# Performance work log

Measured on AMD Instinct MI355X. Metric: run time of the kernel, lower is better.

The kernel has to match this reference:

```python
import jax, jax.numpy as jnp
import numpy as np

N = 50000   # nodes
E = 800000  # edges
G = 64      # graphs in batch
H1, D1 = 2, 64   # gat1: 2 heads x 64
D2 = 32          # gat2: 1 head x 32
IN = 1
EPS = 1e-5


def _gat(h, src, dst, W, al, ar, Wres, bias, Hh, D):
    # DGL GATConv (eval mode): project, per-edge attention, edge softmax over dst, scatter-sum, residual + bias
    feat = (h @ W).reshape(N, Hh, D)                     # [N,H,D]
    el = jnp.sum(feat * al, axis=-1)                     # [N,H]
    er = jnp.sum(feat * ar, axis=-1)                     # [N,H]
    e = jax.nn.leaky_relu(el[src] + er[dst], 0.2)        # [E,H]
    m = jax.ops.segment_max(e, dst, num_segments=N)      # [N,H] (stable softmax)
    a = jnp.exp(e - m[dst])
    s = jax.ops.segment_sum(a, dst, num_segments=N)
    alpha = a / s[dst]                                   # [E,H]
    msg = feat[src] * alpha[:, :, None]                  # [E,H,D]
    rst = jax.ops.segment_sum(msg, dst, num_segments=N)  # [N,H,D]
    res = (h @ Wres).reshape(N, Hh, D)
    return rst + res + bias.reshape(1, Hh, D)


def _bn(x, gamma, beta, mean, var):
    return (x - mean) * jax.lax.rsqrt(var + EPS) * gamma + beta


def setup_inputs() -> dict:
    key = jax.random.key(0)
    ks = jax.random.split(key, 32)
    rn = lambda i, shape: jax.random.normal(ks[i], shape, jnp.float32) * 0.1
    inp = {
        'feat': jax.random.normal(ks[0], (N, IN), jnp.float32),
        'W1': rn(1, (IN, H1 * D1)), 'al1': rn(2, (H1, D1)), 'ar1': rn(3, (H1, D1)),
        'res1': rn(4, (IN, H1 * D1)), 'b1': rn(5, (H1 * D1,)),
        'g1_gamma': jnp.ones((H1 * D1,), jnp.float32), 'g1_beta': jnp.zeros((H1 * D1,), jnp.float32),
        'g1_mean': rn(6, (H1 * D1,)), 'g1_var': jax.random.uniform(ks[7], (H1 * D1,), jnp.float32) + 0.5,
        'W2': rn(8, (H1 * D1, D2)), 'al2': rn(9, (1, D2)), 'ar2': rn(10, (1, D2)),
        'res2': rn(11, (H1 * D1, D2)), 'b2': rn(12, (D2,)),
        'g2_gamma': jnp.ones((D2,), jnp.float32), 'g2_beta': jnp.zeros((D2,), jnp.float32),
        'g2_mean': rn(13, (D2,)), 'g2_var': jax.random.uniform(ks[14], (D2,), jnp.float32) + 0.5,
        'Wd1': rn(15, (D2, H1 * D1)), 'bd1': rn(16, (H1 * D1,)),
        'gd_gamma': jnp.ones((H1 * D1,), jnp.float32), 'gd_beta': jnp.zeros((H1 * D1,), jnp.float32),
        'gd_mean': rn(17, (H1 * D1,)), 'gd_var': jax.random.uniform(ks[18], (H1 * D1,), jnp.float32) + 0.5,
        'Wd2': rn(19, (H1 * D1, IN)), 'bd2': rn(20, (IN,)),
        'src': jax.random.randint(ks[21], (E,), 0, N, jnp.int32),
        'dst': jax.random.randint(ks[22], (E,), 0, N, jnp.int32),
        'graph_ids': jnp.sort(jax.random.randint(ks[23], (N,), 0, G, jnp.int32)),
    }
    return inp


def reference(feat, W1, al1, ar1, res1, b1, g1_gamma, g1_beta, g1_mean, g1_var,
              W2, al2, ar2, res2, b2, g2_gamma, g2_beta, g2_mean, g2_var,
              Wd1, bd1, gd_gamma, gd_beta, gd_mean, gd_var, Wd2, bd2,
              src, dst, graph_ids):
    h = _gat(feat, src, dst, W1, al1, ar1, res1, b1, H1, D1)   # [N,2,64]
    h = h.reshape(N, H1 * D1)
    h = jax.nn.relu(_bn(h, g1_gamma, g1_beta, g1_mean, g1_var))
    h = _gat(h, src, dst, W2, al2, ar2, res2, b2, 1, D2)       # [N,1,32]
    h = h.reshape(N, D2)
    h = jax.nn.relu(_bn(h, g2_gamma, g2_beta, g2_mean, g2_var))
    # dgl.mean_nodes over batched graphs
    counts = jax.ops.segment_sum(jnp.ones((N,), h.dtype), graph_ids, num_segments=G)
    graph_rep = jax.ops.segment_sum(h, graph_ids, num_segments=G) / jnp.maximum(counts, 1.0)[:, None]
    # decoder: Linear -> BN -> ReLU -> Linear (dropout off in eval)
    d = jax.nn.relu(_bn(h @ Wd1 + bd1, gd_gamma, gd_beta, gd_mean, gd_var))
    reconstruction = d @ Wd2 + bd2
    return graph_rep, reconstruction
```

## Files before the change

kernel.cpp:

```cpp
#include <hip/hip_runtime.h>
#include <hip/hip_bf16.h>
#include <hip/hip_fp16.h>

#define NN 50000
#define NE 800000
#define NG 64
#define C1 128
#define D2 32
#define CAP 32
#define RNG 6250
#define NCH 391
#define BN_EPS 1e-5f
#define PREP_BLOCKS 2048

#define CST_A   0
#define CST_B   2
#define CST_P   4
#define CST_Q   132
#define CST_R   260
#define CST_SC2 388
#define CST_RC2 420
#define CST_SD  452
#define CST_RD  580
#define CST_N   1024

#define UO_DEGP  0
#define UO_OVFC  800000
#define UO_WK    800016
#define ZERO_UNITS 800144
#define UO_FLAG  800144
#define UO_CST   800160
#define UO_ESRC2 801184
#define UO_OVF   1601184
#define UO_FCAN  3201184
#define UO_F2    3251184
#define UO_RS2   4051184
#define UO_EL2   5651184
#define UO_ER2   5701184
#define UO_END   5751184

typedef _Float16 h2vec __attribute__((ext_vector_type(2)));

__device__ __forceinline__ float lrelu(float x) { return fmaxf(x, 0.2f * x); }
__device__ __forceinline__ float bu2f(unsigned int u) {
    union { unsigned int i; float f; } v; v.i = (u & 0xFFFFu) << 16; return v.f;
}
__device__ __forceinline__ unsigned short f2bu(float f) {
    union { float f; unsigned int i; } v; v.f = f;
    unsigned int r = v.i + 0x7FFFu + ((v.i >> 16) & 1u);
    return (unsigned short)(r >> 16);
}
__device__ __forceinline__ unsigned int packh2(float a, float b) {
    h2vec h; h.x = (_Float16)a; h.y = (_Float16)b;
    union { h2vec h; unsigned int u; } v; v.h = h; return v.u;
}
__device__ __forceinline__ h2vec as_h2(unsigned int u) {
    union { unsigned int u; h2vec h; } v; v.u = u; return v.h;
}
__device__ __forceinline__ float ldw(const void* p, int i, int bf) {
    return bf ? bu2f(((const unsigned short*)p)[i]) : ((const float*)p)[i];
}
__device__ __forceinline__ int sniff64(const unsigned int* fw, int l) {
    int cnt = 0;
    for (int j = l; j < 256; j += 64) {
        unsigned int b = (fw[j] >> 8) & 0x7Fu;
        cnt += (b >= 0x3Au && b <= 0x41u) ? 1 : 0;
    }
#pragma unroll
    for (int m = 32; m >= 1; m >>= 1) cnt += __shfl_xor(cnt, m);
    return (cnt > 128) ? 1 : 0;
}

__global__ __launch_bounds__(256) void k_prep(
                       const void* __restrict__ feat, const int* __restrict__ dst,
                       const int* __restrict__ src,
                       float* __restrict__ fcan, int* __restrict__ degp,
                       unsigned short* __restrict__ esrc2,
                       int2* __restrict__ ovf, int* __restrict__ ovfc,
                       int* __restrict__ wk,
                       const void* W1, const void* al1, const void* ar1,
                       const void* res1, const void* b1,
                       const void* g1g, const void* g1b, const void* g1m, const void* g1v,
                       const void* b2v, const void* g2g, const void* g2b,
                       const void* g2m, const void* g2v,
                       const void* bd1, const void* gdg, const void* gdb,
                       const void* gdm, const void* gdv,
                       int* __restrict__ flag, float* __restrict__ cst) {
    __shared__ int sBf;
    __shared__ int sC;
    int t = threadIdx.x;
    if (t < 64) {
        int b = sniff64((const unsigned int*)feat, t);
        if (t == 0) sBf = b;
    }
    __syncthreads();
    int bf = sBf;

    if (blockIdx.x == 0) {
        if (t == 0) *flag = bf;
        if (t < 128) {
            if (t < 2) {
                float a = 0.0f, b = 0.0f;
                for (int d = 0; d < 64; ++d) {
                    float w = ldw(W1, t * 64 + d, bf);
                    a += w * ldw(al1, t * 64 + d, bf);
                    b += w * ldw(ar1, t * 64 + d, bf);
                }
                cst[CST_A + t] = a;
                cst[CST_B + t] = b;
            }
            {
                float sc = rsqrtf(ldw(g1v, t, bf) + BN_EPS) * ldw(g1g, t, bf);
                cst[CST_P + t] = ldw(W1, t, bf) * sc;
                cst[CST_Q + t] = ldw(res1, t, bf) * sc;
                cst[CST_R + t] = (ldw(b1, t, bf) - ldw(g1m, t, bf)) * sc + ldw(g1b, t, bf);
            }
            if (t < D2) {
                float sc = rsqrtf(ldw(g2v, t, bf) + BN_EPS) * ldw(g2g, t, bf);
                cst[CST_SC2 + t] = sc;
                cst[CST_RC2 + t] = (ldw(b2v, t, bf) - ldw(g2m, t, bf)) * sc + ldw(g2b, t, bf);
            }
            {
                float sc = rsqrtf(ldw(gdv, t, bf) + BN_EPS) * ldw(gdg, t, bf);
                cst[CST_SD + t] = sc;
                cst[CST_RD + t] = (ldw(bd1, t, bf) - ldw(gdm, t, bf)) * sc + ldw(gdb, t, bf);
            }
        }
    }

    for (int k = blockIdx.x * 256 + t; k < NN; k += PREP_BLOCKS * 256)
        fcan[k] = ldw(feat, k, bf);

    int xcc;
    asm volatile("s_getreg_b32 %0, hwreg(HW_REG_XCC_ID)" : "=s"(xcc));
    xcc &= 7;

    for (int rr = 0; rr < 8; ++rr) {
        int r = (xcc + rr) & 7;
        int lo = r * RNG, hi = lo + RNG;
        for (;;) {
            if (t == 0) sC = atomicAdd(&wk[r * 16], 1);
            __syncthreads();
            int c = sC;
            __syncthreads();
            if (c >= NCH) break;
#pragma unroll
            for (int j = 0; j < 8; ++j) {
                int k = c * 2048 + j * 256 + t;
                if (k < NE) {
                    int d = dst[k];
                    if (d >= lo && d < hi) {
                        int slot = atomicAdd(&degp[d << 4], 1);
                        if (slot < CAP) {
                            esrc2[d * CAP + slot] = (unsigned short)src[k];
                        } else {
                            int p = atomicAdd(ovfc, 1);
                            ovf[p] = make_int2(d, src[k]);
                        }
                    }
                }
            }
        }
    }
}

__global__ __launch_bounds__(256) void k_layer1(
        const float* __restrict__ fcan, const void* W2, const void* res2,
        const void* al2, const void* ar2,
        const int* __restrict__ flag, const float* __restrict__ cst,
        const int* __restrict__ degp, const unsigned short* __restrict__ esrc2,
        const int2* __restrict__ ovf, const int* __restrict__ ovfc,
        unsigned short* __restrict__ F2, float* __restrict__ RS2,
        float* __restrict__ EL2, float* __restrict__ ER2) {
    __shared__ unsigned int sW2pk[32 * 66];
    __shared__ unsigned int sR2pk[32 * 66];
    __shared__ unsigned int sH1pk[32 * 66];
    __shared__ float sP[C1], sQ[C1], sR[C1];
    __shared__ float sAl[D2], sAr[D2];
    int t = threadIdx.x;
    int bf = *flag;
    for (int u = t; u < 2048; u += 256) {
        int cw = u >> 5, l2 = u & 31;
        sW2pk[l2 * 66 + cw] = packh2(ldw(W2, cw * D2 + l2, bf),
                                     ldw(W2, (cw + 64) * D2 + l2, bf));
        sR2pk[l2 * 66 + cw] = packh2(ldw(res2, cw * D2 + l2, bf),
                                     ldw(res2, (cw + 64) * D2 + l2, bf));
    }
    if (t < C1) { sP[t] = cst[CST_P + t]; sQ[t] = cst[CST_Q + t]; sR[t] = cst[CST_R + t]; }
    if (t < D2) { sAl[t] = ldw(al2, t, bf); sAr[t] = ldw(ar2, t, bf); }
    __syncthreads();

    int l = t & 31;
    int g = t >> 5;
    int base = blockIdx.x * 32;
    float A0 = cst[CST_A + 0], A1 = cst[CST_A + 1];
    float B0 = cst[CST_B + 0], B1 = cst[CST_B + 1];

    int dcap[4], draw[4];
    float fiK[4];
#pragma unroll
    for (int k = 0; k < 4; ++k) {
        int i = base + g * 4 + k;
        if (i < NN) {
            draw[k] = degp[i << 4];
            dcap[k] = draw[k] < CAP ? draw[k] : CAP;
            fiK[k] = fcan[i];
        } else { draw[k] = 0; dcap[k] = 0; fiK[k] = 0.0f; }
    }
    float S0[4], S1[4], N0[4], N1[4];
#pragma unroll
    for (int k = 0; k < 4; ++k) { S0[k] = S1[k] = N0[k] = N1[k] = 0.0f; }
    int sA[4];
#pragma unroll
    for (int k = 0; k < 4; ++k)
        sA[k] = (l < dcap[k]) ? (int)esrc2[(base + g * 4 + k) * CAP + l] : 0;
    float fA[4];
#pragma unroll
    for (int k = 0; k < 4; ++k) fA[k] = fcan[sA[k]];
#pragma unroll
    for (int k = 0; k < 4; ++k) {
        if (l < dcap[k]) {
            float w0 = __expf(lrelu(A0 * fA[k] + B0 * fiK[k]));
            float w1 = __expf(lrelu(A1 * fA[k] + B1 * fiK[k]));
            S0[k] += w0; N0[k] += w0 * fA[k];
            S1[k] += w1; N1[k] += w1 * fA[k];
        }
    }
#pragma unroll
    for (int k = 0; k < 4; ++k) {
        if (draw[k] > CAP) {
            int i = base + g * 4 + k;
            int novf = *ovfc;
            for (int p = l; p < novf; p += 32) {
                int2 o = ovf[p];
                if (o.x == i) {
                    float fs = fcan[o.y];
                    float w0 = __expf(lrelu(A0 * fs + B0 * fiK[k]));
                    float w1 = __expf(lrelu(A1 * fs + B1 * fiK[k]));
                    S0[k] += w0; N0[k] += w0 * fs;
                    S1[k] += w1; N1[k] += w1 * fs;
                }
            }
        }
    }
#pragma unroll
    for (int m = 16; m >= 1; m >>= 1) {
#pragma unroll
        for (int k = 0; k < 4; ++k) {
            S0[k] += __shfl_xor(S0[k], m); N0[k] += __shfl_xor(N0[k], m);
            S1[k] += __shfl_xor(S1[k], m); N1[k] += __shfl_xor(N1[k], m);
        }
    }
#pragma unroll
    for (int k = 0; k < 4; ++k) {
        int slot = g * 4 + k;
        float T0 = S0[k] > 0.0f ? N0[k] / S0[k] : 0.0f;
        float T1 = S1[k] > 0.0f ? N1[k] / S1[k] : 0.0f;
        float h0  = fmaxf(sP[l]      * T0 + sQ[l]      * fiK[k] + sR[l],      0.0f);
        float h1v = fmaxf(sP[l + 32] * T0 + sQ[l + 32] * fiK[k] + sR[l + 32], 0.0f);
        float h2v = fmaxf(sP[l + 64] * T1 + sQ[l + 64] * fiK[k] + sR[l + 64], 0.0f);
        float h3v = fmaxf(sP[l + 96] * T1 + sQ[l + 96] * fiK[k] + sR[l + 96], 0.0f);
        sH1pk[slot * 66 + l]      = packh2(h0,  h2v);
        sH1pk[slot * 66 + l + 32] = packh2(h1v, h3v);
    }
    __syncthreads();

    int w = t >> 6;
    int half = (t >> 5) & 1;
    int nb0 = w * 8 + half * 4;
    float aF[4] = {0.f, 0.f, 0.f, 0.f}, aR[4] = {0.f, 0.f, 0.f, 0.f};
    for (int cw = 0; cw < 64; cw += 2) {
        uint2 wq = *(const uint2*)&sW2pk[l * 66 + cw];
        uint2 rq = *(const uint2*)&sR2pk[l * 66 + cw];
#pragma unroll
        for (int n = 0; n < 4; ++n) {
            uint2 hq = *(const uint2*)&sH1pk[(nb0 + n) * 66 + cw];
            aF[n] = __builtin_amdgcn_fdot2(as_h2(hq.x), as_h2(wq.x),
                    __builtin_amdgcn_fdot2(as_h2(hq.y), as_h2(wq.y), aF[n], false), false);
            aR[n] = __builtin_amdgcn_fdot2(as_h2(hq.x), as_h2(rq.x),
                    __builtin_amdgcn_fdot2(as_h2(hq.y), as_h2(rq.y), aR[n], false), false);
        }
    }
#pragma unroll
    for (int n = 0; n < 4; ++n) {
        int i = base + nb0 + n;
        if (i < NN) {
            float elp = aF[n] * sAl[l], erp = aF[n] * sAr[l];
#pragma unroll
            for (int m = 16; m >= 1; m >>= 1) {
                elp += __shfl_xor(elp, m);
                erp += __shfl_xor(erp, m);
            }
            if (l == 0) { EL2[i] = elp; ER2[i] = erp; }
            F2[(size_t)i * D2 + l]  = f2bu(aF[n]);
            RS2[(size_t)i * D2 + l] = aR[n];
        }
    }
}

__global__ __launch_bounds__(256, 8) void k_final(
        const void* Wd1, const void* Wd2, const void* bd2,
        const int* __restrict__ flag, const float* __restrict__ cst,
        const int* __restrict__ degp, const unsigned short* __restrict__ esrc2,
        const int2* __restrict__ ovf, const int* __restrict__ ovfc,
        const unsigned short* __restrict__ F2, float* __restrict__ RS2,
        const float* __restrict__ EL2, const float* __restrict__ ER2,
        float* __restrict__ out) {
    __shared__ float sWd1x[4096];
    __shared__ unsigned int sWS[8 * 64];
    int t = threadIdx.x;
    int bf = *flag;
    for (int u = t; u < 4096; u += 256) {
        int d = u >> 7, lq = (u >> 2) & 31, j = u & 3;
        sWd1x[u] = ldw(Wd1, d * C1 + j * 32 + lq, bf);
    }

    int i = (blockIdx.x * 256 + t) >> 5;
    int l = t & 31;
    int nb = t >> 5;

    float sc2 = cst[CST_SC2 + l], rc2 = cst[CST_RC2 + l];
    float sd0 = cst[CST_SD + l],      rd0 = cst[CST_RD + l];
    float sd1 = cst[CST_SD + l + 32], rd1 = cst[CST_RD + l + 32];
    float sd2 = cst[CST_SD + l + 64], rd2 = cst[CST_RD + l + 64];
    float sd3 = cst[CST_SD + l + 96], rd3 = cst[CST_RD + l + 96];
    float wd2_0 = ldw(Wd2, l, bf),      wd2_1 = ldw(Wd2, l + 32, bf);
    float wd2_2 = ldw(Wd2, l + 64, bf), wd2_3 = ldw(Wd2, l + 96, bf);
    __syncthreads();

    float eri = ER2[i];
    int dr = degp[i << 4];
    int dcap = dr < CAP ? dr : CAP;
    const unsigned short* row = &esrc2[i * CAP];

    int sMy = 0; float wMy = 0.0f;
    if (l < dcap) {
        sMy = (int)row[l];
        wMy = __expf(lrelu(EL2[sMy] + eri));
    }
    float S = wMy;
#pragma unroll
    for (int m = 16; m >= 1; m >>= 1) S += __shfl_xor(S, m);
    sWS[nb * 64 + 2 * l]     = __float_as_uint(wMy);
    sWS[nb * 64 + 2 * l + 1] = (unsigned int)sMy;

    float aF0 = 0.f, aF1 = 0.f, aF2 = 0.f, aF3 = 0.f;
    int e = 0;
    for (; e + 3 < dcap; e += 4) {
        uint2 p0 = *(const uint2*)&sWS[nb * 64 + 2 * e];
        uint2 p1 = *(const uint2*)&sWS[nb * 64 + 2 * (e + 1)];
        uint2 p2 = *(const uint2*)&sWS[nb * 64 + 2 * (e + 2)];
        uint2 p3 = *(const uint2*)&sWS[nb * 64 + 2 * (e + 3)];
        float v0 = bu2f(F2[(size_t)p0.y * D2 + l]);
        float v1 = bu2f(F2[(size_t)p1.y * D2 + l]);
        float v2 = bu2f(F2[(size_t)p2.y * D2 + l]);
        float v3 = bu2f(F2[(size_t)p3.y * D2 + l]);
        aF0 = fmaf(__uint_as_float(p0.x), v0, aF0);
        aF1 = fmaf(__uint_as_float(p1.x), v1, aF1);
        aF2 = fmaf(__uint_as_float(p2.x), v2, aF2);
        aF3 = fmaf(__uint_as_float(p3.x), v3, aF3);
    }
    for (; e < dcap; ++e) {
        uint2 p = *(const uint2*)&sWS[nb * 64 + 2 * e];
        aF0 = fmaf(__uint_as_float(p.x), bu2f(F2[(size_t)p.y * D2 + l]), aF0);
    }
    if (dr > CAP) {
        int novf = *ovfc;
        for (int p = 0; p < novf; ++p) {
            int2 o = ovf[p];
            if (o.x == i) {
                float wA = __expf(lrelu(EL2[o.y] + eri));
                S += wA;
                aF0 = fmaf(wA, bu2f(F2[(size_t)o.y * D2 + l]), aF0);
            }
        }
    }
    float aF = (aF0 + aF1) + (aF2 + aF3);
    float inv = S > 0.0f ? 1.0f / S : 0.0f;

    float h2 = fmaxf((aF * inv + RS2[(size_t)i * D2 + l]) * sc2 + rc2, 0.0f);
    RS2[(size_t)i * D2 + l] = h2;

    const float4* Wx = (const float4*)sWd1x;
    float ac0 = 0.0f, ac1 = 0.0f, ac2 = 0.0f, ac3 = 0.0f;
#pragma unroll
    for (int d = 0; d < D2; ++d) {
        float h = __shfl(h2, d, 32);
        float4 wv = Wx[d * 32 + l];
        ac0 = fmaf(h, wv.x, ac0);
        ac1 = fmaf(h, wv.y, ac1);
        ac2 = fmaf(h, wv.z, ac2);
        ac3 = fmaf(h, wv.w, ac3);
    }
    float rec = fmaxf(ac0 * sd0 + rd0, 0.0f) * wd2_0
              + fmaxf(ac1 * sd1 + rd1, 0.0f) * wd2_1
              + fmaxf(ac2 * sd2 + rd2, 0.0f) * wd2_2
              + fmaxf(ac3 * sd3 + rd3, 0.0f) * wd2_3;
#pragma unroll
    for (int m = 16; m >= 1; m >>= 1) rec += __shfl_xor(rec, m);
    if (l == 0) out[NG * D2 + i] = rec + ldw(bd2, 0, bf);
}

__global__ __launch_bounds__(256) void k_pool2(const int* __restrict__ gid,
                                               const float* __restrict__ H2,
                                               float* __restrict__ out) {
    __shared__ int sLo, sHi;
    __shared__ float sAcc[32 * 32];
    int g = blockIdx.x >> 2;
    int part = blockIdx.x & 3;
    int t = threadIdx.x;
    if (t == 0) {
        int lo = 0, hi = NN;
        while (lo < hi) { int m = (lo + hi) >> 1; if (gid[m] < g) lo = m + 1; else hi = m; }
        sLo = lo;
        lo = 0; hi = NN;
        while (lo < hi) { int m = (lo + hi) >> 1; if (gid[m] < g + 1) lo = m + 1; else hi = m; }
        sHi = lo;
    }
    __syncthreads();
    int lo = sLo, hi = sHi;
    int q = t & 7;
    int row = t >> 3;
    float4 acc = make_float4(0.f, 0.f, 0.f, 0.f);
    for (int i = lo + part * 32 + row; i < hi; i += 128) {
        float4 v = ((const float4*)&H2[(size_t)i * D2])[q];
        acc.x += v.x; acc.y += v.y; acc.z += v.z; acc.w += v.w;
    }
    *(float4*)&sAcc[row * 32 + 4 * q] = acc;
    __syncthreads();
    if (t < 32) {
        float a = 0.0f;
        for (int r = 0; r < 32; ++r) a += sAcc[r * 32 + t];
        float inv = 1.0f / fmaxf((float)(hi - lo), 1.0f);
        atomicAdd(&out[g * D2 + t], a * inv);
    }
}

extern "C" void kernel_launch(void* const* d_in, const int* in_sizes, int n_in,
                              void* d_out, int out_size, void* d_ws, size_t ws_size,
                              hipStream_t stream) {
    const void* feat = d_in[0];
    const void* W1 = d_in[1];  const void* al1 = d_in[2];  const void* ar1 = d_in[3];
    const void* res1 = d_in[4]; const void* b1 = d_in[5];
    const void* g1g = d_in[6]; const void* g1b = d_in[7];
    const void* g1m = d_in[8]; const void* g1v = d_in[9];
    const void* W2 = d_in[10]; const void* al2 = d_in[11]; const void* ar2 = d_in[12];
    const void* res2 = d_in[13]; const void* b2v = d_in[14];
    const void* g2g = d_in[15]; const void* g2b = d_in[16];
    const void* g2m = d_in[17]; const void* g2v = d_in[18];
    const void* Wd1 = d_in[19]; const void* bd1 = d_in[20];
    const void* gdg = d_in[21]; const void* gdb = d_in[22];
    const void* gdm = d_in[23]; const void* gdv = d_in[24];
    const void* Wd2 = d_in[25]; const void* bd2 = d_in[26];
    const int* src = (const int*)d_in[27];
    const int* dst = (const int*)d_in[28];
    const int* gid = (const int*)d_in[29];

    unsigned int* wsu = (unsigned int*)d_ws;
    int* degp   = (int*)(wsu + UO_DEGP);
    int* ovfc   = (int*)(wsu + UO_OVFC);
    int* wk     = (int*)(wsu + UO_WK);
    int* flag   = (int*)(wsu + UO_FLAG);
    float* cst  = (float*)(wsu + UO_CST);
    unsigned short* esrc2 = (unsigned short*)(wsu + UO_ESRC2);
    int2* ovf   = (int2*)(wsu + UO_OVF);
    float* fcan = (float*)(wsu + UO_FCAN);
    unsigned short* F2 = (unsigned short*)(wsu + UO_F2);
    float* RS2  = (float*)(wsu + UO_RS2);
    float* EL2  = (float*)(wsu + UO_EL2);
    float* ER2  = (float*)(wsu + UO_ER2);

    hipMemsetAsync(d_ws, 0, (size_t)ZERO_UNITS * 4, stream);
    hipMemsetAsync(d_out, 0, (size_t)NG * D2 * sizeof(float), stream);

    k_prep<<<PREP_BLOCKS, 256, 0, stream>>>(feat, dst, src, fcan, degp,
                                            esrc2, ovf, ovfc, wk,
                                            W1, al1, ar1, res1, b1,
                                            g1g, g1b, g1m, g1v,
                                            b2v, g2g, g2b, g2m, g2v,
                                            bd1, gdg, gdb, gdm, gdv,
                                            flag, cst);

    k_layer1<<<(NN + 31) / 32, 256, 0, stream>>>(fcan, W2, res2, al2, ar2, flag, cst,
                                                 degp, esrc2, ovf, ovfc,
                                                 F2, RS2, EL2, ER2);

    k_final<<<(NN * 32) / 256, 256, 0, stream>>>(Wd1, Wd2, bd2, flag, cst,
                                                 degp, esrc2, ovf, ovfc,
                                                 F2, RS2, EL2, ER2,
                                                 (float*)d_out);

    k_pool2<<<NG * 4, 256, 0, stream>>>(gid, RS2, (float*)d_out);
}
```

Before: 284.3 us.

## Fuse all stages into one cooperative persistent kernel with grid syncs

```diff
diff --git a/kernel.cpp b/kernel.cpp
--- a/kernel.cpp
+++ b/kernel.cpp
@@ -1,6 +1,9 @@
 #include <hip/hip_runtime.h>
 #include <hip/hip_bf16.h>
 #include <hip/hip_fp16.h>
+#include <hip/hip_cooperative_groups.h>
+
+namespace cg = cooperative_groups;
 
 #define NN 50000
 #define NE 800000
@@ -11,7 +14,7 @@
 #define RNG 6250
 #define NCH 391
 #define BN_EPS 1e-5f
-#define PREP_BLOCKS 2048
+#define FGRID 1024
 
 #define CST_A   0
 #define CST_B   2
@@ -26,20 +29,38 @@
 
 #define UO_DEGP  0
 #define UO_OVFC  800000
-#define UO_WK    800016
-#define ZERO_UNITS 800144
-#define UO_FLAG  800144
-#define UO_CST   800160
-#define UO_ESRC2 801184
-#define UO_OVF   1601184
-#define UO_FCAN  3201184
-#define UO_F2    3251184
-#define UO_RS2   4051184
-#define UO_EL2   5651184
-#define UO_ER2   5701184
-#define UO_END   5751184
+#define ZERO_UNITS 800016
+#define UO_CST   800016
+#define UO_ESRC2 801040
+#define UO_OVF   1601040
+#define UO_FCAN  3201040
+#define UO_F2    3251040
+#define UO_RS2   4051040
+#define UO_EL2   5651040
+#define UO_ER2   5701040
 
 typedef _Float16 h2vec __attribute__((ext_vector_type(2)));
+
+struct Params {
+    const void *feat, *W1, *al1, *ar1, *res1, *b1, *g1g, *g1b, *g1m, *g1v;
+    const void *W2, *al2, *ar2, *res2, *b2v, *g2g, *g2b, *g2m, *g2v;
+    const void *Wd1, *bd1, *gdg, *gdb, *gdm, *gdv, *Wd2, *bd2;
+    const int *src, *dst, *gid;
+    unsigned int *wsz;
+    int *degp, *ovfc;
+    float *cst, *fcan;
+    unsigned short *esrc2;
+    int2 *ovf;
+    unsigned short *F2;
+    float *RS2, *EL2, *ER2, *out;
+};
+
+union SMem {
+    struct { unsigned int W2pk[32 * 66], R2pk[32 * 66], H1pk[32 * 66];
+             float P[C1], Q[C1], R[C1], Al[D2], Ar[D2]; } l1;
+    struct { float Wd1x[4096]; unsigned int WS[8 * 64]; } fin;
+    struct { float Acc[32 * 32]; int Lo, Hi; } pool;
+};
 
 __device__ __forceinline__ float lrelu(float x) { return fmaxf(x, 0.2f * x); }
 __device__ __forceinline__ float bu2f(unsigned int u) {
@@ -70,93 +91,51 @@
     for (int m = 32; m >= 1; m >>= 1) cnt += __shfl_xor(cnt, m);
     return (cnt > 128) ? 1 : 0;
 }
-
-__global__ __launch_bounds__(256) void k_prep(
-                       const void* __restrict__ feat, const int* __restrict__ dst,
-                       const int* __restrict__ src,
-                       float* __restrict__ fcan, int* __restrict__ degp,
-                       unsigned short* __restrict__ esrc2,
-                       int2* __restrict__ ovf, int* __restrict__ ovfc,
-                       int* __restrict__ wk,
-                       const void* W1, const void* al1, const void* ar1,
-                       const void* res1, const void* b1,
-                       const void* g1g, const void* g1b, const void* g1m, const void* g1v,
-                       const void* b2v, const void* g2g, const void* g2b,
-                       const void* g2m, const void* g2v,
-                       const void* bd1, const void* gdg, const void* gdb,
-                       const void* gdm, const void* gdv,
-                       int* __restrict__ flag, float* __restrict__ cst) {
-    __shared__ int sBf;
-    __shared__ int sC;
-    int t = threadIdx.x;
-    if (t < 64) {
-        int b = sniff64((const unsigned int*)feat, t);
-        if (t == 0) sBf = b;
-    }
+__device__ __forceinline__ int block_bf(const void* feat, int t, int* sBf) {
+    if (t < 64) { int b = sniff64((const unsigned int*)feat, t); if (t == 0) *sBf = b; }
     __syncthreads();
-    int bf = sBf;
-
-    if (blockIdx.x == 0) {
-        if (t == 0) *flag = bf;
-        if (t < 128) {
-            if (t < 2) {
-                float a = 0.0f, b = 0.0f;
-                for (int d = 0; d < 64; ++d) {
-                    float w = ldw(W1, t * 64 + d, bf);
-                    a += w * ldw(al1, t * 64 + d, bf);
-                    b += w * ldw(ar1, t * 64 + d, bf);
-                }
-                cst[CST_A + t] = a;
-                cst[CST_B + t] = b;
-            }
-            {
-                float sc = rsqrtf(ldw(g1v, t, bf) + BN_EPS) * ldw(g1g, t, bf);
-                cst[CST_P + t] = ldw(W1, t, bf) * sc;
-                cst[CST_Q + t] = ldw(res1, t, bf) * sc;
-                cst[CST_R + t] = (ldw(b1, t, bf) - ldw(g1m, t, bf)) * sc + ldw(g1b, t, bf);
-            }
-            if (t < D2) {
-                float sc = rsqrtf(ldw(g2v, t, bf) + BN_EPS) * ldw(g2g, t, bf);
-                cst[CST_SC2 + t] = sc;
-                cst[CST_RC2 + t] = (ldw(b2v, t, bf) - ldw(g2m, t, bf)) * sc + ldw(g2b, t, bf);
-            }
-            {
-                float sc = rsqrtf(ldw(gdv, t, bf) + BN_EPS) * ldw(gdg, t, bf);
-                cst[CST_SD + t] = sc;
-                cst[CST_RD + t] = (ldw(bd1, t, bf) - ldw(gdm, t, bf)) * sc + ldw(gdb, t, bf);
-            }
-        }
-    }
-
-    for (int k = blockIdx.x * 256 + t; k < NN; k += PREP_BLOCKS * 256)
-        fcan[k] = ldw(feat, k, bf);
-
-    int xcc;
-    asm volatile("s_getreg_b32 %0, hwreg(HW_REG_XCC_ID)" : "=s"(xcc));
-    xcc &= 7;
-
-    for (int rr = 0; rr < 8; ++rr) {
-        int r = (xcc + rr) & 7;
+    return *sBf;
+}
+
+__device__ __forceinline__ void dev_fold(const Params& p, int t, int bf) {
+    if (t < 128) {
+        float w1v = ldw(p.W1, t, bf);
+        float pa = w1v * ldw(p.al1, t, bf);
+        float pb = w1v * ldw(p.ar1, t, bf);
+#pragma unroll
+        for (int m = 32; m >= 1; m >>= 1) { pa += __shfl_xor(pa, m); pb += __shfl_xor(pb, m); }
+        if ((t & 63) == 0) { p.cst[CST_A + (t >> 6)] = pa; p.cst[CST_B + (t >> 6)] = pb; }
+        float sc = rsqrtf(ldw(p.g1v, t, bf) + BN_EPS) * ldw(p.g1g, t, bf);
+        p.cst[CST_P + t] = w1v * sc;
+        p.cst[CST_Q + t] = ldw(p.res1, t, bf) * sc;
+        p.cst[CST_R + t] = (ldw(p.b1, t, bf) - ldw(p.g1m, t, bf)) * sc + ldw(p.g1b, t, bf);
+        if (t < D2) {
+            float s2 = rsqrtf(ldw(p.g2v, t, bf) + BN_EPS) * ldw(p.g2g, t, bf);
+            p.cst[CST_SC2 + t] = s2;
+            p.cst[CST_RC2 + t] = (ldw(p.b2v, t, bf) - ldw(p.g2m, t, bf)) * s2 + ldw(p.g2b, t, bf);
+        }
+        float sd = rsqrtf(ldw(p.gdv, t, bf) + BN_EPS) * ldw(p.gdg, t, bf);
+        p.cst[CST_SD + t] = sd;
+        p.cst[CST_RD + t] = (ldw(p.bd1, t, bf) - ldw(p.gdm, t, bf)) * sd + ldw(p.gdb, t, bf);
+    }
+}
+
+__device__ __forceinline__ void dev_prep(const Params& p, int bid, int nbk, int t) {
+    for (int idx = bid; idx < NCH * 8; idx += nbk) {
+        int r = idx & 7, c = idx >> 3;
         int lo = r * RNG, hi = lo + RNG;
-        for (;;) {
-            if (t == 0) sC = atomicAdd(&wk[r * 16], 1);
-            __syncthreads();
-            int c = sC;
-            __syncthreads();
-            if (c >= NCH) break;
-#pragma unroll
-            for (int j = 0; j < 8; ++j) {
-                int k = c * 2048 + j * 256 + t;
-                if (k < NE) {
-                    int d = dst[k];
-                    if (d >= lo && d < hi) {
-                        int slot = atomicAdd(&degp[d << 4], 1);
-                        if (slot < CAP) {
-                            esrc2[d * CAP + slot] = (unsigned short)src[k];
-                        } else {
-                            int p = atomicAdd(ovfc, 1);
-                            ovf[p] = make_int2(d, src[k]);
-                        }
+#pragma unroll
+        for (int j = 0; j < 8; ++j) {
+            int k = c * 2048 + j * 256 + t;
+            if (k < NE) {
+                int d = p.dst[k];
+                if (d >= lo && d < hi) {
+                    int slot = atomicAdd(&p.degp[d << 4], 1);
+                    if (slot < CAP) {
+                        p.esrc2[d * CAP + slot] = (unsigned short)p.src[k];
+                    } else {
+                        int q = atomicAdd(p.ovfc, 1);
+                        p.ovf[q] = make_int2(d, p.src[k]);
                     }
                 }
             }
@@ -164,331 +143,341 @@
     }
 }
 
-__global__ __launch_bounds__(256) void k_layer1(
-        const float* __restrict__ fcan, const void* W2, const void* res2,
-        const void* al2, const void* ar2,
-        const int* __restrict__ flag, const float* __restrict__ cst,
-        const int* __restrict__ degp, const unsigned short* __restrict__ esrc2,
-        const int2* __restrict__ ovf, const int* __restrict__ ovfc,
-        unsigned short* __restrict__ F2, float* __restrict__ RS2,
-        float* __restrict__ EL2, float* __restrict__ ER2) {
-    __shared__ unsigned int sW2pk[32 * 66];
-    __shared__ unsigned int sR2pk[32 * 66];
-    __shared__ unsigned int sH1pk[32 * 66];
-    __shared__ float sP[C1], sQ[C1], sR[C1];
-    __shared__ float sAl[D2], sAr[D2];
-    int t = threadIdx.x;
-    int bf = *flag;
+__device__ void dev_layer1(const Params& p, SMem& sm, int bid, int nbk, int t, int bf) {
     for (int u = t; u < 2048; u += 256) {
         int cw = u >> 5, l2 = u & 31;
-        sW2pk[l2 * 66 + cw] = packh2(ldw(W2, cw * D2 + l2, bf),
-                                     ldw(W2, (cw + 64) * D2 + l2, bf));
-        sR2pk[l2 * 66 + cw] = packh2(ldw(res2, cw * D2 + l2, bf),
-                                     ldw(res2, (cw + 64) * D2 + l2, bf));
-    }
-    if (t < C1) { sP[t] = cst[CST_P + t]; sQ[t] = cst[CST_Q + t]; sR[t] = cst[CST_R + t]; }
-    if (t < D2) { sAl[t] = ldw(al2, t, bf); sAr[t] = ldw(ar2, t, bf); }
+        sm.l1.W2pk[l2 * 66 + cw] = packh2(ldw(p.W2, cw * D2 + l2, bf),
+                                          ldw(p.W2, (cw + 64) * D2 + l2, bf));
+        sm.l1.R2pk[l2 * 66 + cw] = packh2(ldw(p.res2, cw * D2 + l2, bf),
+                                          ldw(p.res2, (cw + 64) * D2 + l2, bf));
+    }
+    if (t < C1) { sm.l1.P[t] = p.cst[CST_P + t]; sm.l1.Q[t] = p.cst[CST_Q + t]; sm.l1.R[t] = p.cst[CST_R + t]; }
+    if (t < D2) { sm.l1.Al[t] = ldw(p.al2, t, bf); sm.l1.Ar[t] = ldw(p.ar2, t, bf); }
+    float A0 = p.cst[CST_A + 0], A1 = p.cst[CST_A + 1];
+    float B0 = p.cst[CST_B + 0], B1 = p.cst[CST_B + 1];
     __syncthreads();
 
-    int l = t & 31;
-    int g = t >> 5;
-    int base = blockIdx.x * 32;
-    float A0 = cst[CST_A + 0], A1 = cst[CST_A + 1];
-    float B0 = cst[CST_B + 0], B1 = cst[CST_B + 1];
-
-    int dcap[4], draw[4];
-    float fiK[4];
-#pragma unroll
-    for (int k = 0; k < 4; ++k) {
-        int i = base + g * 4 + k;
-        if (i < NN) {
-            draw[k] = degp[i << 4];
-            dcap[k] = draw[k] < CAP ? draw[k] : CAP;
-            fiK[k] = fcan[i];
-        } else { draw[k] = 0; dcap[k] = 0; fiK[k] = 0.0f; }
-    }
-    float S0[4], S1[4], N0[4], N1[4];
-#pragma unroll
-    for (int k = 0; k < 4; ++k) { S0[k] = S1[k] = N0[k] = N1[k] = 0.0f; }
-    int sA[4];
-#pragma unroll
-    for (int k = 0; k < 4; ++k)
-        sA[k] = (l < dcap[k]) ? (int)esrc2[(base + g * 4 + k) * CAP + l] : 0;
-    float fA[4];
-#pragma unroll
-    for (int k = 0; k < 4; ++k) fA[k] = fcan[sA[k]];
-#pragma unroll
-    for (int k = 0; k < 4; ++k) {
-        if (l < dcap[k]) {
-            float w0 = __expf(lrelu(A0 * fA[k] + B0 * fiK[k]));
-            float w1 = __expf(lrelu(A1 * fA[k] + B1 * fiK[k]));
-            S0[k] += w0; N0[k] += w0 * fA[k];
-            S1[k] += w1; N1[k] += w1 * fA[k];
-        }
-    }
-#pragma unroll
-    for (int k = 0; k < 4; ++k) {
-        if (draw[k] > CAP) {
+    int l = t & 31, g = t >> 5;
+    int w = t >> 6, half = (t >> 5) & 1, nb0 = w * 8 + half * 4;
+
+    for (int base = bid * 32; base < NN; base += nbk * 32) {
+        int dcap[4], draw[4];
+        float fiK[4];
+#pragma unroll
+        for (int k = 0; k < 4; ++k) {
             int i = base + g * 4 + k;
-            int novf = *ovfc;
-            for (int p = l; p < novf; p += 32) {
-                int2 o = ovf[p];
-                if (o.x == i) {
-                    float fs = fcan[o.y];
-                    float w0 = __expf(lrelu(A0 * fs + B0 * fiK[k]));
-                    float w1 = __expf(lrelu(A1 * fs + B1 * fiK[k]));
-                    S0[k] += w0; N0[k] += w0 * fs;
-                    S1[k] += w1; N1[k] += w1 * fs;
+            if (i < NN) {
+                draw[k] = p.degp[i << 4];
+                dcap[k] = draw[k] < CAP ? draw[k] : CAP;
+                fiK[k] = p.fcan[i];
+            } else { draw[k] = 0; dcap[k] = 0; fiK[k] = 0.0f; }
+        }
+        float S0[4], S1[4], N0[4], N1[4];
+#pragma unroll
+        for (int k = 0; k < 4; ++k) { S0[k] = S1[k] = N0[k] = N1[k] = 0.0f; }
+        int sA[4];
+#pragma unroll
+        for (int k = 0; k < 4; ++k)
+            sA[k] = (l < dcap[k]) ? (int)p.esrc2[(base + g * 4 + k) * CAP + l] : 0;
+        float fA[4];
+#pragma unroll
+        for (int k = 0; k < 4; ++k) fA[k] = p.fcan[sA[k]];
+#pragma unroll
+        for (int k = 0; k < 4; ++k) {
+            if (l < dcap[k]) {
+                float w0 = __expf(lrelu(A0 * fA[k] + B0 * fiK[k]));
+                float w1 = __expf(lrelu(A1 * fA[k] + B1 * fiK[k]));
+                S0[k] += w0; N0[k] += w0 * fA[k];
+                S1[k] += w1; N1[k] += w1 * fA[k];
+            }
+        }
+#pragma unroll
+        for (int k = 0; k < 4; ++k) {
+            if (draw[k] > CAP) {
+                int i = base + g * 4 + k;
+                int novf = *p.ovfc;
+                for (int q = l; q < novf; q += 32) {
+                    int2 o = p.ovf[q];
+                    if (o.x == i) {
+                        float fs = p.fcan[o.y];
+                        float w0 = __expf(lrelu(A0 * fs + B0 * fiK[k]));
+                        float w1 = __expf(lrelu(A1 * fs + B1 * fiK[k]));
+                        S0[k] += w0; N0[k] += w0 * fs;
+                        S1[k] += w1; N1[k] += w1 * fs;
+                    }
                 }
             }
         }
-    }
-#pragma unroll
-    for (int m = 16; m >= 1; m >>= 1) {
+#pragma unroll
+        for (int m = 16; m >= 1; m >>= 1) {
+#pragma unroll
+            for (int k = 0; k < 4; ++k) {
+                S0[k] += __shfl_xor(S0[k], m); N0[k] += __shfl_xor(N0[k], m);
+                S1[k] += __shfl_xor(S1[k], m); N1[k] += __shfl_xor(N1[k], m);
+            }
+        }
 #pragma unroll
         for (int k = 0; k < 4; ++k) {
-            S0[k] += __shfl_xor(S0[k], m); N0[k] += __shfl_xor(N0[k], m);
-            S1[k] += __shfl_xor(S1[k], m); N1[k] += __shfl_xor(N1[k], m);
-        }
-    }
-#pragma unroll
-    for (int k = 0; k < 4; ++k) {
-        int slot = g * 4 + k;
-        float T0 = S0[k] > 0.0f ? N0[k] / S0[k] : 0.0f;
-        float T1 = S1[k] > 0.0f ? N1[k] / S1[k] : 0.0f;
-        float h0  = fmaxf(sP[l]      * T0 + sQ[l]      * fiK[k] + sR[l],      0.0f);
-        float h1v = fmaxf(sP[l + 32] * T0 + sQ[l + 32] * fiK[k] + sR[l + 32], 0.0f);
-        float h2v = fmaxf(sP[l + 64] * T1 + sQ[l + 64] * fiK[k] + sR[l + 64], 0.0f);
-        float h3v = fmaxf(sP[l + 96] * T1 + sQ[l + 96] * fiK[k] + sR[l + 96], 0.0f);
-        sH1pk[slot * 66 + l]      = packh2(h0,  h2v);
-        sH1pk[slot * 66 + l + 32] = packh2(h1v, h3v);
-    }
-    __syncthreads();
-
-    int w = t >> 6;
-    int half = (t >> 5) & 1;
-    int nb0 = w * 8 + half * 4;
-    float aF[4] = {0.f, 0.f, 0.f, 0.f}, aR[4] = {0.f, 0.f, 0.f, 0.f};
-    for (int cw = 0; cw < 64; cw += 2) {
-        uint2 wq = *(const uint2*)&sW2pk[l * 66 + cw];
-        uint2 rq = *(const uint2*)&sR2pk[l * 66 + cw];
+            int slot = g * 4 + k;
+            float T0 = S0[k] > 0.0f ? N0[k] / S0[k] : 0.0f;
+            float T1 = S1[k] > 0.0f ? N1[k] / S1[k] : 0.0f;
+            float h0  = fmaxf(sm.l1.P[l]      * T0 + sm.l1.Q[l]      * fiK[k] + sm.l1.R[l],      0.0f);
+            float h1v = fmaxf(sm.l1.P[l + 32] * T0 + sm.l1.Q[l + 32] * fiK[k] + sm.l1.R[l + 32], 0.0f);
+            float h2v = fmaxf(sm.l1.P[l + 64] * T1 + sm.l1.Q[l + 64] * fiK[k] + sm.l1.R[l + 64], 0.0f);
+            float h3v = fmaxf(sm.l1.P[l + 96] * T1 + sm.l1.Q[l + 96] * fiK[k] + sm.l1.R[l + 96], 0.0f);
+            sm.l1.H1pk[slot * 66 + l]      = packh2(h0,  h2v);
+            sm.l1.H1pk[slot * 66 + l + 32] = packh2(h1v, h3v);
+        }
+        __syncthreads();
+
+        float aF[4] = {0.f, 0.f, 0.f, 0.f}, aR[4] = {0.f, 0.f, 0.f, 0.f};
+        for (int cw = 0; cw < 64; cw += 2) {
+            uint2 wq = *(const uint2*)&sm.l1.W2pk[l * 66 + cw];
+            uint2 rq = *(const uint2*)&sm.l1.R2pk[l * 66 + cw];
+#pragma unroll
+            for (int n = 0; n < 4; ++n) {
+                uint2 hq = *(const uint2*)&sm.l1.H1pk[(nb0 + n) * 66 + cw];
+                aF[n] = __builtin_amdgcn_fdot2(as_h2(hq.x), as_h2(wq.x),
+                        __builtin_amdgcn_fdot2(as_h2(hq.y), as_h2(wq.y), aF[n], false), false);
+                aR[n] = __builtin_amdgcn_fdot2(as_h2(hq.x), as_h2(rq.x),
+                        __builtin_amdgcn_fdot2(as_h2(hq.y), as_h2(rq.y), aR[n], false), false);
+            }
+        }
 #pragma unroll
         for (int n = 0; n < 4; ++n) {
-            uint2 hq = *(const uint2*)&sH1pk[(nb0 + n) * 66 + cw];
-            aF[n] = __builtin_amdgcn_fdot2(as_h2(hq.x), as_h2(wq.x),
-                    __builtin_amdgcn_fdot2(as_h2(hq.y), as_h2(wq.y), aF[n], false), false);
-            aR[n] = __builtin_amdgcn_fdot2(as_h2(hq.x), as_h2(rq.x),
-                    __builtin_amdgcn_fdot2(as_h2(hq.y), as_h2(rq.y), aR[n], false), false);
-        }
-    }
-#pragma unroll
-    for (int n = 0; n < 4; ++n) {
-        int i = base + nb0 + n;
-        if (i < NN) {
-            float elp = aF[n] * sAl[l], erp = aF[n] * sAr[l];
-#pragma unroll
-            for (int m = 16; m >= 1; m >>= 1) {
-                elp += __shfl_xor(elp, m);
-                erp += __shfl_xor(erp, m);
-            }
-            if (l == 0) { EL2[i] = elp; ER2[i] = erp; }
-            F2[(size_t)i * D2 + l]  = f2bu(aF[n]);
-            RS2[(size_t)i * D2 + l] = aR[n];
-        }
-    }
-}
-
-__global__ __launch_bounds__(256, 8) void k_final(
-        const void* Wd1, const void* Wd2, const void* bd2,
-        const int* __restrict__ flag, const float* __restrict__ cst,
-        const int* __restrict__ degp, const unsigned short* __restrict__ esrc2,
-        const int2* __restrict__ ovf, const int* __restrict__ ovfc,
-        const unsigned short* __restrict__ F2, float* __restrict__ RS2,
-        const float* __restrict__ EL2, const float* __restrict__ ER2,
-        float* __restrict__ out) {
-    __shared__ float sWd1x[4096];
-    __shared__ unsigned int sWS[8 * 64];
-    int t = threadIdx.x;
-    int bf = *flag;
+            int i = base + nb0 + n;
+            if (i < NN) {
+                float elp = aF[n] * sm.l1.Al[l], erp = aF[n] * sm.l1.Ar[l];
+#pragma unroll
+                for (int m = 16; m >= 1; m >>= 1) {
+                    elp += __shfl_xor(elp, m);
+                    erp += __shfl_xor(erp, m);
+                }
+                if (l == 0) { p.EL2[i] = elp; p.ER2[i] = erp; }
+                p.F2[(size_t)i * D2 + l]  = f2bu(aF[n]);
+                p.RS2[(size_t)i * D2 + l] = aR[n];
+            }
+        }
+        __syncthreads();
+    }
+}
+
+__device__ void dev_final(const Params& p, SMem& sm, int bid, int nbk, int t, int bf) {
     for (int u = t; u < 4096; u += 256) {
         int d = u >> 7, lq = (u >> 2) & 31, j = u & 3;
-        sWd1x[u] = ldw(Wd1, d * C1 + j * 32 + lq, bf);
-    }
-
-    int i = (blockIdx.x * 256 + t) >> 5;
+        sm.fin.Wd1x[u] = ldw(p.Wd1, d * C1 + j * 32 + lq, bf);
+    }
     int l = t & 31;
-    int nb = t >> 5;
-
-    float sc2 = cst[CST_SC2 + l], rc2 = cst[CST_RC2 + l];
-    float sd0 = cst[CST_SD + l],      rd0 = cst[CST_RD + l];
-    float sd1 = cst[CST_SD + l + 32], rd1 = cst[CST_RD + l + 32];
-    float sd2 = cst[CST_SD + l + 64], rd2 = cst[CST_RD + l + 64];
-    float sd3 = cst[CST_SD + l + 96], rd3 = cst[CST_RD + l + 96];
-    float wd2_0 = ldw(Wd2, l, bf),      wd2_1 = ldw(Wd2, l + 32, bf);
-    float wd2_2 = ldw(Wd2, l + 64, bf), wd2_3 = ldw(Wd2, l + 96, bf);
+    int ng = t >> 5;
+    float sc2 = p.cst[CST_SC2 + l], rc2 = p.cst[CST_RC2 + l];
+    float sd0 = p.cst[CST_SD + l],      rd0 = p.cst[CST_RD + l];
+    float sd1 = p.cst[CST_SD + l + 32], rd1 = p.cst[CST_RD + l + 32];
+    float sd2 = p.cst[CST_SD + l + 64], rd2 = p.cst[CST_RD + l + 64];
+    float sd3 = p.cst[CST_SD + l + 96], rd3 = p.cst[CST_RD + l + 96];
+    float wd2_0 = ldw(p.Wd2, l, bf),      wd2_1 = ldw(p.Wd2, l + 32, bf);
+    float wd2_2 = ldw(p.Wd2, l + 64, bf), wd2_3 = ldw(p.Wd2, l + 96, bf);
+    float bd2v  = ldw(p.bd2, 0, bf);
     __syncthreads();
 
-    float eri = ER2[i];
-    int dr = degp[i << 4];
-    int dcap = dr < CAP ? dr : CAP;
-    const unsigned short* row = &esrc2[i * CAP];
-
-    int sMy = 0; float wMy = 0.0f;
-    if (l < dcap) {
-        sMy = (int)row[l];
-        wMy = __expf(lrelu(EL2[sMy] + eri));
-    }
-    float S = wMy;
-#pragma unroll
-    for (int m = 16; m >= 1; m >>= 1) S += __shfl_xor(S, m);
-    sWS[nb * 64 + 2 * l]     = __float_as_uint(wMy);
-    sWS[nb * 64 + 2 * l + 1] = (unsigned int)sMy;
-
-    float aF0 = 0.f, aF1 = 0.f, aF2 = 0.f, aF3 = 0.f;
-    int e = 0;
-    for (; e + 3 < dcap; e += 4) {
-        uint2 p0 = *(const uint2*)&sWS[nb * 64 + 2 * e];
-        uint2 p1 = *(const uint2*)&sWS[nb * 64 + 2 * (e + 1)];
-        uint2 p2 = *(const uint2*)&sWS[nb * 64 + 2 * (e + 2)];
-        uint2 p3 = *(const uint2*)&sWS[nb * 64 + 2 * (e + 3)];
-        float v0 = bu2f(F2[(size_t)p0.y * D2 + l]);
-        float v1 = bu2f(F2[(size_t)p1.y * D2 + l]);
-        float v2 = bu2f(F2[(size_t)p2.y * D2 + l]);
-        float v3 = bu2f(F2[(size_t)p3.y * D2 + l]);
-        aF0 = fmaf(__uint_as_float(p0.x), v0, aF0);
-        aF1 = fmaf(__uint_as_float(p1.x), v1, aF1);
-        aF2 = fmaf(__uint_as_float(p2.x), v2, aF2);
-        aF3 = fmaf(__uint_as_float(p3.x), v3, aF3);
-    }
-    for (; e < dcap; ++e) {
-        uint2 p = *(const uint2*)&sWS[nb * 64 + 2 * e];
-        aF0 = fmaf(__uint_as_float(p.x), bu2f(F2[(size_t)p.y * D2 + l]), aF0);
-    }
-    if (dr > CAP) {
-        int novf = *ovfc;
-        for (int p = 0; p < novf; ++p) {
-            int2 o = ovf[p];
-            if (o.x == i) {
-                float wA = __expf(lrelu(EL2[o.y] + eri));
-                S += wA;
-                aF0 = fmaf(wA, bu2f(F2[(size_t)o.y * D2 + l]), aF0);
-            }
-        }
-    }
-    float aF = (aF0 + aF1) + (aF2 + aF3);
-    float inv = S > 0.0f ? 1.0f / S : 0.0f;
-
-    float h2 = fmaxf((aF * inv + RS2[(size_t)i * D2 + l]) * sc2 + rc2, 0.0f);
-    RS2[(size_t)i * D2 + l] = h2;
-
-    const float4* Wx = (const float4*)sWd1x;
-    float ac0 = 0.0f, ac1 = 0.0f, ac2 = 0.0f, ac3 = 0.0f;
-#pragma unroll
-    for (int d = 0; d < D2; ++d) {
-        float h = __shfl(h2, d, 32);
-        float4 wv = Wx[d * 32 + l];
-        ac0 = fmaf(h, wv.x, ac0);
-        ac1 = fmaf(h, wv.y, ac1);
-        ac2 = fmaf(h, wv.z, ac2);
-        ac3 = fmaf(h, wv.w, ac3);
-    }
-    float rec = fmaxf(ac0 * sd0 + rd0, 0.0f) * wd2_0
-              + fmaxf(ac1 * sd1 + rd1, 0.0f) * wd2_1
-              + fmaxf(ac2 * sd2 + rd2, 0.0f) * wd2_2
-              + fmaxf(ac3 * sd3 + rd3, 0.0f) * wd2_3;
-#pragma unroll
-    for (int m = 16; m >= 1; m >>= 1) rec += __shfl_xor(rec, m);
-    if (l == 0) out[NG * D2 + i] = rec + ldw(bd2, 0, bf);
-}
-
-__global__ __launch_bounds__(256) void k_pool2(const int* __restrict__ gid,
-                                               const float* __restrict__ H2,
-                                               float* __restrict__ out) {
-    __shared__ int sLo, sHi;
-    __shared__ float sAcc[32 * 32];
-    int g = blockIdx.x >> 2;
-    int part = blockIdx.x & 3;
+    const float4* Wx = (const float4*)sm.fin.Wd1x;
+    for (int i0 = bid * 8; i0 < NN; i0 += nbk * 8) {
+        int i = i0 + ng;
+        float eri = p.ER2[i];
+        int dr = p.degp[i << 4];
+        int dcap = dr < CAP ? dr : CAP;
+        const unsigned short* row = &p.esrc2[i * CAP];
+
+        int sMy = 0; float wMy = 0.0f;
+        if (l < dcap) {
+            sMy = (int)row[l];
+            wMy = __expf(lrelu(p.EL2[sMy] + eri));
+        }
+        float S = wMy;
+#pragma unroll
+        for (int m = 16; m >= 1; m >>= 1) S += __shfl_xor(S, m);
+        sm.fin.WS[ng * 64 + 2 * l]     = __float_as_uint(wMy);
+        sm.fin.WS[ng * 64 + 2 * l + 1] = (unsigned int)sMy;
+
+        float aF0 = 0.f, aF1 = 0.f, aF2 = 0.f, aF3 = 0.f;
+        int e = 0;
+        for (; e + 3 < dcap; e += 4) {
+            uint2 p0 = *(const uint2*)&sm.fin.WS[ng * 64 + 2 * e];
+            uint2 p1 = *(const uint2*)&sm.fin.WS[ng * 64 + 2 * (e + 1)];
+            uint2 p2 = *(const uint2*)&sm.fin.WS[ng * 64 + 2 * (e + 2)];
+            uint2 p3 = *(const uint2*)&sm.fin.WS[ng * 64 + 2 * (e + 3)];
+            float v0 = bu2f(p.F2[(size_t)p0.y * D2 + l]);
+            float v1 = bu2f(p.F2[(size_t)p1.y * D2 + l]);
+            float v2 = bu2f(p.F2[(size_t)p2.y * D2 + l]);
+            float v3 = bu2f(p.F2[(size_t)p3.y * D2 + l]);
+            aF0 = fmaf(__uint_as_float(p0.x), v0, aF0);
+            aF1 = fmaf(__uint_as_float(p1.x), v1, aF1);
+            aF2 = fmaf(__uint_as_float(p2.x), v2, aF2);
+            aF3 = fmaf(__uint_as_float(p3.x), v3, aF3);
+        }
+        for (; e < dcap; ++e) {
+            uint2 pr = *(const uint2*)&sm.fin.WS[ng * 64 + 2 * e];
+            aF0 = fmaf(__uint_as_float(pr.x), bu2f(p.F2[(size_t)pr.y * D2 + l]), aF0);
+        }
+        if (dr > CAP) {
+            int novf = *p.ovfc;
+            for (int q = 0; q < novf; ++q) {
+                int2 o = p.ovf[q];
+                if (o.x == i) {
+                    float wA = __expf(lrelu(p.EL2[o.y] + eri));
+                    S += wA;
+                    aF0 = fmaf(wA, bu2f(p.F2[(size_t)o.y * D2 + l]), aF0);
+                }
+            }
+        }
+        float aF = (aF0 + aF1) + (aF2 + aF3);
+        float inv = S > 0.0f ? 1.0f / S : 0.0f;
+
+        float h2 = fmaxf((aF * inv + p.RS2[(size_t)i * D2 + l]) * sc2 + rc2, 0.0f);
+        p.RS2[(size_t)i * D2 + l] = h2;
+
+        float ac0 = 0.0f, ac1 = 0.0f, ac2 = 0.0f, ac3 = 0.0f;
+#pragma unroll
+        for (int d = 0; d < D2; ++d) {
+            float h = __shfl(h2, d, 32);
+            float4 wv = Wx[d * 32 + l];
+            ac0 = fmaf(h, wv.x, ac0);
+            ac1 = fmaf(h, wv.y, ac1);
+            ac2 = fmaf(h, wv.z, ac2);
+            ac3 = fmaf(h, wv.w, ac3);
+        }
+        float rec = fmaxf(ac0 * sd0 + rd0, 0.0f) * wd2_0
+                  + fmaxf(ac1 * sd1 + rd1, 0.0f) * wd2_1
+                  + fmaxf(ac2 * sd2 + rd2, 0.0f) * wd2_2
+                  + fmaxf(ac3 * sd3 + rd3, 0.0f) * wd2_3;
+#pragma unroll
+        for (int m = 16; m >= 1; m >>= 1) rec += __shfl_xor(rec, m);
+        if (l == 0) p.out[NG * D2 + i] = rec + bd2v;
+    }
+}
+
+__device__ void dev_pool(const Params& p, SMem& sm, int bid, int nbk, int t) {
+    for (int job = bid; job < NG * 4; job += nbk) {
+        int g = job >> 2, part = job & 3;
+        if (t == 0) {
+            int lo = 0, hi = NN;
+            while (lo < hi) { int m = (lo + hi) >> 1; if (p.gid[m] < g) lo = m + 1; else hi = m; }
+            sm.pool.Lo = lo;
+            lo = 0; hi = NN;
+            while (lo < hi) { int m = (lo + hi) >> 1; if (p.gid[m] < g + 1) lo = m + 1; else hi = m; }
+            sm.pool.Hi = lo;
+        }
+        __syncthreads();
+        int lo = sm.pool.Lo, hi = sm.pool.Hi;
+        int q = t & 7, row = t >> 3;
+        float4 acc = make_float4(0.f, 0.f, 0.f, 0.f);
+        for (int i = lo + part * 32 + row; i < hi; i += 128) {
+            float4 v = ((const float4*)&p.RS2[(size_t)i * D2])[q];
+            acc.x += v.x; acc.y += v.y; acc.z += v.z; acc.w += v.w;
+        }
+        *(float4*)&sm.pool.Acc[row * 32 + 4 * q] = acc;
+        __syncthreads();
+        if (t < 32) {
+            float a = 0.0f;
+            for (int r = 0; r < 32; ++r) a += sm.pool.Acc[r * 32 + t];
+            atomicAdd(&p.out[g * D2 + t], a / fmaxf((float)(hi - lo), 1.0f));
+        }
+        __syncthreads();
+    }
+}
+
+__global__ __launch_bounds__(256, 4) void k_fused(Params p) {
+    cg::grid_group gg = cg::this_grid();
+    __shared__ SMem sm;
+    __shared__ int sBf;
+    int t = threadIdx.x, bid = blockIdx.x, nbk = gridDim.x;
+    int bf = block_bf(p.feat, t, &sBf);
+
+    for (int u = bid * 256 + t; u < ZERO_UNITS; u += nbk * 256) p.wsz[u] = 0u;
+    for (int u = bid * 256 + t; u < NG * D2; u += nbk * 256) p.out[u] = 0.0f;
+    for (int k = bid * 256 + t; k < NN; k += nbk * 256) p.fcan[k] = ldw(p.feat, k, bf);
+    if (bid == 0) dev_fold(p, t, bf);
+    gg.sync();
+
+    dev_prep(p, bid, nbk, t);
+    gg.sync();
+
+    dev_layer1(p, sm, bid, nbk, t, bf);
+    gg.sync();
+
+    dev_final(p, sm, bid, nbk, t, bf);
+    gg.sync();
+
+    dev_pool(p, sm, bid, nbk, t);
+}
+
+__global__ __launch_bounds__(256) void k_prep_l(Params p) {
+    __shared__ int sBf;
     int t = threadIdx.x;
-    if (t == 0) {
-        int lo = 0, hi = NN;
-        while (lo < hi) { int m = (lo + hi) >> 1; if (gid[m] < g) lo = m + 1; else hi = m; }
-        sLo = lo;
-        lo = 0; hi = NN;
-        while (lo < hi) { int m = (lo + hi) >> 1; if (gid[m] < g + 1) lo = m + 1; else hi = m; }
-        sHi = lo;
-    }
-    __syncthreads();
-    int lo = sLo, hi = sHi;
-    int q = t & 7;
-    int row = t >> 3;
-    float4 acc = make_float4(0.f, 0.f, 0.f, 0.f);
-    for (int i = lo + part * 32 + row; i < hi; i += 128) {
-        float4 v = ((const float4*)&H2[(size_t)i * D2])[q];
-        acc.x += v.x; acc.y += v.y; acc.z += v.z; acc.w += v.w;
-    }
-    *(float4*)&sAcc[row * 32 + 4 * q] = acc;
-    __syncthreads();
-    if (t < 32) {
-        float a = 0.0f;
-        for (int r = 0; r < 32; ++r) a += sAcc[r * 32 + t];
-        float inv = 1.0f / fmaxf((float)(hi - lo), 1.0f);
-        atomicAdd(&out[g * D2 + t], a * inv);
-    }
+    int bf = block_bf(p.feat, t, &sBf);
+    if (blockIdx.x == 0) dev_fold(p, t, bf);
+    for (int k = blockIdx.x * 256 + t; k < NN; k += gridDim.x * 256) p.fcan[k] = ldw(p.feat, k, bf);
+    dev_prep(p, blockIdx.x, gridDim.x, t);
+}
+__global__ __launch_bounds__(256) void k_layer1_l(Params p) {
+    __shared__ SMem sm;
+    __shared__ int sBf;
+    int t = threadIdx.x;
+    int bf = block_bf(p.feat, t, &sBf);
+    dev_layer1(p, sm, blockIdx.x, gridDim.x, t, bf);
+}
+__global__ __launch_bounds__(256) void k_final_l(Params p) {
+    __shared__ SMem sm;
+    __shared__ int sBf;
+    int t = threadIdx.x;
+    int bf = block_bf(p.feat, t, &sBf);
+    dev_final(p, sm, blockIdx.x, gridDim.x, t, bf);
+}
+__global__ __launch_bounds__(256) void k_pool_l(Params p) {
+    __shared__ SMem sm;
+    dev_pool(p, sm, blockIdx.x, gridDim.x, threadIdx.x);
 }
 
 extern "C" void kernel_launch(void* const* d_in, const int* in_sizes, int n_in,
                               void* d_out, int out_size, void* d_ws, size_t ws_size,
                               hipStream_t stream) {
-    const void* feat = d_in[0];
-    const void* W1 = d_in[1];  const void* al1 = d_in[2];  const void* ar1 = d_in[3];
-    const void* res1 = d_in[4]; const void* b1 = d_in[5];
-    const void* g1g = d_in[6]; const void* g1b = d_in[7];
-    const void* g1m = d_in[8]; const void* g1v = d_in[9];
-    const void* W2 = d_in[10]; const void* al2 = d_in[11]; const void* ar2 = d_in[12];
-    const void* res2 = d_in[13]; const void* b2v = d_in[14];
-    const void* g2g = d_in[15]; const void* g2b = d_in[16];
-    const void* g2m = d_in[17]; const void* g2v = d_in[18];
-    const void* Wd1 = d_in[19]; const void* bd1 = d_in[20];
-    const void* gdg = d_in[21]; const void* gdb = d_in[22];
-    const void* gdm = d_in[23]; const void* gdv = d_in[24];
-    const void* Wd2 = d_in[25]; const void* bd2 = d_in[26];
-    const int* src = (const int*)d_in[27];
-    const int* dst = (const int*)d_in[28];
-    const int* gid = (const int*)d_in[29];
-
     unsigned int* wsu = (unsigned int*)d_ws;
-    int* degp   = (int*)(wsu + UO_DEGP);
-    int* ovfc   = (int*)(wsu + UO_OVFC);
-    int* wk     = (int*)(wsu + UO_WK);
-    int* flag   = (int*)(wsu + UO_FLAG);
-    float* cst  = (float*)(wsu + UO_CST);
-    unsigned short* esrc2 = (unsigned short*)(wsu + UO_ESRC2);
-    int2* ovf   = (int2*)(wsu + UO_OVF);
-    float* fcan = (float*)(wsu + UO_FCAN);
-    unsigned short* F2 = (unsigned short*)(wsu + UO_F2);
-    float* RS2  = (float*)(wsu + UO_RS2);
-    float* EL2  = (float*)(wsu + UO_EL2);
-    float* ER2  = (float*)(wsu + UO_ER2);
-
-    hipMemsetAsync(d_ws, 0, (size_t)ZERO_UNITS * 4, stream);
-    hipMemsetAsync(d_out, 0, (size_t)NG * D2 * sizeof(float), stream);
-
-    k_prep<<<PREP_BLOCKS, 256, 0, stream>>>(feat, dst, src, fcan, degp,
-                                            esrc2, ovf, ovfc, wk,
-                                            W1, al1, ar1, res1, b1,
-                                            g1g, g1b, g1m, g1v,
-                                            b2v, g2g, g2b, g2m, g2v,
-                                            bd1, gdg, gdb, gdm, gdv,
-                                            flag, cst);
-
-    k_layer1<<<(NN + 31) / 32, 256, 0, stream>>>(fcan, W2, res2, al2, ar2, flag, cst,
-                                                 degp, esrc2, ovf, ovfc,
-                                                 F2, RS2, EL2, ER2);
-
-    k_final<<<(NN * 32) / 256, 256, 0, stream>>>(Wd1, Wd2, bd2, flag, cst,
-                                                 degp, esrc2, ovf, ovfc,
-                                                 F2, RS2, EL2, ER2,
-                                                 (float*)d_out);
-
-    k_pool2<<<NG * 4, 256, 0, stream>>>(gid, RS2, (float*)d_out);
-}
+    Params prm;
+    prm.feat = d_in[0];
+    prm.W1 = d_in[1];  prm.al1 = d_in[2];  prm.ar1 = d_in[3];
+    prm.res1 = d_in[4]; prm.b1 = d_in[5];
+    prm.g1g = d_in[6]; prm.g1b = d_in[7]; prm.g1m = d_in[8]; prm.g1v = d_in[9];
+    prm.W2 = d_in[10]; prm.al2 = d_in[11]; prm.ar2 = d_in[12];
+    prm.res2 = d_in[13]; prm.b2v = d_in[14];
+    prm.g2g = d_in[15]; prm.g2b = d_in[16]; prm.g2m = d_in[17]; prm.g2v = d_in[18];
+    prm.Wd1 = d_in[19]; prm.bd1 = d_in[20];
+    prm.gdg = d_in[21]; prm.gdb = d_in[22]; prm.gdm = d_in[23]; prm.gdv = d_in[24];
+    prm.Wd2 = d_in[25]; prm.bd2 = d_in[26];
+    prm.src = (const int*)d_in[27];
+    prm.dst = (const int*)d_in[28];
+    prm.gid = (const int*)d_in[29];
+    prm.wsz   = wsu;
+    prm.degp  = (int*)(wsu + UO_DEGP);
+    prm.ovfc  = (int*)(wsu + UO_OVFC);
+    prm.cst   = (float*)(wsu + UO_CST);
+    prm.esrc2 = (unsigned short*)(wsu + UO_ESRC2);
+    prm.ovf   = (int2*)(wsu + UO_OVF);
+    prm.fcan  = (float*)(wsu + UO_FCAN);
+    prm.F2    = (unsigned short*)(wsu + UO_F2);
+    prm.RS2   = (float*)(wsu + UO_RS2);
+    prm.EL2   = (float*)(wsu + UO_EL2);
+    prm.ER2   = (float*)(wsu + UO_ER2);
+    prm.out   = (float*)d_out;
+
+    void* ka[] = { (void*)&prm };
+    hipError_t err = hipLaunchCooperativeKernel((const void*)k_fused,
+                                                dim3(FGRID), dim3(256), ka, 0, stream);
+    if (err != hipSuccess) {
+        (void)hipGetLastError();
+        hipMemsetAsync(d_ws, 0, (size_t)ZERO_UNITS * 4, stream);
+        hipMemsetAsync(d_out, 0, (size_t)NG * D2 * sizeof(float), stream);
+        k_prep_l<<<NCH * 8, 256, 0, stream>>>(prm);
+        k_layer1_l<<<(NN + 31) / 32, 256, 0, stream>>>(prm);
+        k_final_l<<<NN / 8, 256, 0, stream>>>(prm);
+        k_pool_l<<<NG * 4, 256, 0, stream>>>(prm);
+    }
+}
```

After: 735.9 us. +158.8%, slower.
